# Optimization experiments

Measured on AMD Instinct MI355X. Metric: run time of the kernel, lower is better.

The kernel has to match this reference:

```python
import jax, jax.numpy as jnp
import numpy as np

B, S, E, H = 4, 2048, 2048, 16
HD = E // H  # 128
SCALE = 1.0 / float(np.sqrt(HD))


def setup_inputs() -> dict:
    key = jax.random.key(0)
    ks = jax.random.split(key, 9)
    std = 0.02
    return {
        "QKV": jax.random.normal(ks[0], (B, S, E), dtype=jnp.float32),
        "Wq": jax.random.normal(ks[1], (E, E), dtype=jnp.float32) * std,
        "bq": jnp.zeros((E,), dtype=jnp.float32),
        "Wk": jax.random.normal(ks[2], (E, E), dtype=jnp.float32) * std,
        "bk": jnp.zeros((E,), dtype=jnp.float32),
        "Wv": jax.random.normal(ks[3], (E, E), dtype=jnp.float32) * std,
        "bv": jnp.zeros((E,), dtype=jnp.float32),
        "Wo": jax.random.normal(ks[4], (E, E), dtype=jnp.float32) * std,
        "bo": jnp.zeros((E,), dtype=jnp.float32),
        "is_causal": 1,
    }


def _split_heads(x):
    # [B,S,E] -> [B,H,S,HD]
    return x.reshape(B, -1, H, HD).transpose(0, 2, 1, 3)


def reference(QKV, Wq, bq, Wk, bk, Wv, bv, Wo, bo, is_causal):
    # nn.Linear: y = x @ W.T + b
    Q = _split_heads(QKV @ Wq.T + bq)
    K = _split_heads(QKV @ Wk.T + bk)
    V = _split_heads(QKV @ Wv.T + bv)
    P = jnp.einsum("bhqd,bhkd->bhqk", Q, K) * SCALE
    # FAITHFUL: original masked_fill uses (ones_like(...) == 0) -> all-False
    # mask, so causal masking is a no-op regardless of is_causal.
    P = jax.nn.softmax(P, axis=-1)
    out = jnp.einsum("bhqk,bhkd->bhqd", P, V)
    out = out.transpose(0, 2, 1, 3).reshape(B, -1, E)  # [B,S,E]
    return out @ Wo.T + bo
```

## Files before the change

kernel.cpp:

```cpp
#include <hip/hip_runtime.h>
#include <stdint.h>

#define BB 4
#define SS 2048
#define EE 2048
#define HH 16
#define HD 128
#define QSCALE 0.1275174490044696f

typedef __attribute__((ext_vector_type(8))) short bf16x8;
typedef __attribute__((ext_vector_type(4))) float f32x4;

__device__ __forceinline__ unsigned short f2bf(float f) {
  union { float f; unsigned u; } v;
  v.f = f;
  unsigned r = (v.u + 0x7fffu + ((v.u >> 16) & 1u)) >> 16;
  return (unsigned short)r;
}
__device__ __forceinline__ float bf2f(unsigned short u) {
  union { unsigned u; float f; } v;
  v.u = ((unsigned)u) << 16;
  return v.f;
}

__device__ __forceinline__ void lds16(const void* g, void* l) {
  __builtin_amdgcn_global_load_lds(
      (__attribute__((address_space(1))) void*)(uintptr_t)g,
      (__attribute__((address_space(3))) void*)(uintptr_t)l,
      16, 0, 0);
}

__global__ void cvt_f32_bf16(const float* __restrict__ src,
                             unsigned short* __restrict__ dst, int n4) {
  int i = blockIdx.x * blockDim.x + threadIdx.x;
  if (i >= n4) return;
  float4 v = ((const float4*)src)[i];
  ushort4 o;
  o.x = f2bf(v.x); o.y = f2bf(v.y); o.z = f2bf(v.z); o.w = f2bf(v.w);
  ((ushort4*)dst)[i] = o;
}

__global__ void cvt_w3(const float* __restrict__ Wq,
                       const float* __restrict__ Wk,
                       const float* __restrict__ Wv,
                       unsigned short* __restrict__ dst, int n4each) {
  const int which = blockIdx.y;
  const float* src = (which == 0) ? Wq : (which == 1) ? Wk : Wv;
  unsigned short* d = dst + (size_t)which * 4194304;
  int i = blockIdx.x * blockDim.x + threadIdx.x;
  if (i >= n4each) return;
  float4 v = ((const float4*)src)[i];
  ushort4 o;
  o.x = f2bf(v.x); o.y = f2bf(v.y); o.z = f2bf(v.z); o.w = f2bf(v.w);
  ((ushort4*)d)[i] = o;
}

__device__ __forceinline__ void gemm_bt_core(const unsigned short* __restrict__ A,
                                             const unsigned short* __restrict__ Bm,
                                             unsigned short* As, unsigned short* Bs,
                                             int m0, int n0, int K, f32x4 acc[4][4]) {
  const int t = threadIdx.x;
  const int w = t >> 6;
  const int lr = t & 15;
  const int lg = (t & 63) >> 4;
  const int wm = (w >> 1) * 64;
  const int wn = (w & 1) * 64;

  const unsigned short* Ag0 = A + (size_t)(m0 + (t >> 2)) * K + (t & 3) * 8;
  const unsigned short* Ag1 = Ag0 + (size_t)64 * K;
  const unsigned short* Bg0 = Bm + (size_t)(n0 + (t >> 2)) * K + (t & 3) * 8;
  const unsigned short* Bg1 = Bg0 + (size_t)64 * K;
  char* AsB = (char*)As + (w * 64) * 16;
  char* BsB = (char*)Bs + (w * 64) * 16;

#pragma unroll
  for (int i = 0; i < 4; ++i)
#pragma unroll
    for (int j = 0; j < 4; ++j)
      acc[i][j] = (f32x4){0.f, 0.f, 0.f, 0.f};

  for (int kt = 0; kt < K; kt += 32) {
    lds16(Ag0 + kt, AsB);
    lds16(Ag1 + kt, AsB + 256 * 16);
    lds16(Bg0 + kt, BsB);
    lds16(Bg1 + kt, BsB + 256 * 16);
    __syncthreads();
    bf16x8 af[4], bf[4];
#pragma unroll
    for (int i = 0; i < 4; ++i)
      af[i] = *(const bf16x8*)(As + (wm + i * 16 + lr) * 32 + lg * 8);
#pragma unroll
    for (int j = 0; j < 4; ++j)
      bf[j] = *(const bf16x8*)(Bs + (wn + j * 16 + lr) * 32 + lg * 8);
#pragma unroll
    for (int i = 0; i < 4; ++i)
#pragma unroll
      for (int j = 0; j < 4; ++j)
        acc[i][j] = __builtin_amdgcn_mfma_f32_16x16x32_bf16(af[i], bf[j], acc[i][j], 0, 0, 0);
    __syncthreads();
  }
}

__global__ __launch_bounds__(256, 2)
void gemm_qkv(const unsigned short* __restrict__ X,
              const unsigned short* __restrict__ W,
              const float* __restrict__ bq,
              const float* __restrict__ bk,
              const float* __restrict__ bv,
              unsigned short* __restrict__ Qb,
              unsigned short* __restrict__ Kb,
              unsigned short* __restrict__ Vb) {
  __shared__ __align__(16) unsigned short As[128 * 32];
  __shared__ __align__(16) unsigned short Bs[128 * 32];
  const int m0 = blockIdx.y * 128;
  const int n0 = blockIdx.x * 128;
  f32x4 acc[4][4];
  gemm_bt_core(X, W, As, Bs, m0, n0, EE, acc);

  const int t = threadIdx.x;
  const int w = t >> 6;
  const int lr = t & 15;
  const int lg = (t & 63) >> 4;
  const int wm = (w >> 1) * 64;
  const int wn = (w & 1) * 64;

  const int region = n0 >> 11;
  unsigned short* Dst = (region == 0) ? Qb : (region == 1) ? Kb : Vb;
  const float* bp = (region == 0) ? bq : (region == 1) ? bk : bv;

  if (region == 2) {
#pragma unroll
    for (int i = 0; i < 4; ++i) {
      const int row0 = m0 + wm + i * 16 + lg * 4;
      const int b = row0 >> 11;
      const int s = row0 & 2047;
#pragma unroll
      for (int j = 0; j < 4; ++j) {
        const int c = (n0 + wn + j * 16 + lr) & 2047;
        const float bias = bp[c];
        const int h = c >> 7, hd = c & 127;
        const size_t base = ((size_t)(b * HH + h) * HD + hd) * SS + s;
#pragma unroll
        for (int re = 0; re < 4; ++re)
          Dst[base + re] = f2bf(acc[i][j][re] + bias);
      }
    }
  } else {
    const float osc = (region == 0) ? QSCALE : 1.0f;
#pragma unroll
    for (int i = 0; i < 4; ++i) {
      const int row0 = m0 + wm + i * 16 + lg * 4;
      const int b = row0 >> 11;
      const int s = row0 & 2047;
#pragma unroll
      for (int j = 0; j < 4; ++j) {
        const int c = (n0 + wn + j * 16 + lr) & 2047;
        const float bias = bp[c];
        const int h = c >> 7, hd = c & 127;
        const size_t base = ((size_t)(b * HH + h) * SS + s) * HD + hd;
#pragma unroll
        for (int re = 0; re < 4; ++re)
          Dst[base + (size_t)re * HD] = f2bf((acc[i][j][re] + bias) * osc);
      }
    }
  }
}

__global__ __launch_bounds__(256, 2)
void gemm_out(const unsigned short* __restrict__ A,
              const unsigned short* __restrict__ W,
              const float* __restrict__ bo,
              float* __restrict__ Out) {
  __shared__ __align__(16) unsigned short As[128 * 32];
  __shared__ __align__(16) unsigned short Bs[128 * 32];
  const int m0 = blockIdx.y * 128;
  const int n0 = blockIdx.x * 128;
  f32x4 acc[4][4];
  gemm_bt_core(A, W, As, Bs, m0, n0, EE, acc);

  const int t = threadIdx.x;
  const int w = t >> 6;
  const int lr = t & 15;
  const int lg = (t & 63) >> 4;
  const int wm = (w >> 1) * 64;
  const int wn = (w & 1) * 64;

#pragma unroll
  for (int i = 0; i < 4; ++i) {
    const int row0 = m0 + wm + i * 16 + lg * 4;
#pragma unroll
    for (int j = 0; j < 4; ++j) {
      const int col = n0 + wn + j * 16 + lr;
      const float bias = bo[col];
#pragma unroll
      for (int re = 0; re < 4; ++re)
        Out[(size_t)(row0 + re) * EE + col] = acc[i][j][re] + bias;
    }
  }
}

__global__ __launch_bounds__(256, 2)
void attn_mfma(const unsigned short* __restrict__ Qb,
               const unsigned short* __restrict__ Kb,
               const unsigned short* __restrict__ Vtb,
               unsigned short* __restrict__ At) {
  __shared__ __align__(16) char lds[81920];
  const int t = threadIdx.x;
  const int w = t >> 6;
  const int ln = t & 63;
  const int lr = ln & 15;
  const int lg = ln >> 4;
  char* Ps = lds + 65536 + w * 4096;

  const int bh = blockIdx.y;
  const int qw = blockIdx.x * 128 + w * 32;

  const unsigned short* Qh = Qb + (size_t)bh * SS * HD;
  const unsigned short* Kh = Kb + (size_t)bh * SS * HD;
  const unsigned short* Vh = Vtb + (size_t)bh * HD * SS;

  bf16x8 qfr[2][4];
#pragma unroll
  for (int qi = 0; qi < 2; ++qi)
#pragma unroll
    for (int ds = 0; ds < 4; ++ds)
      qfr[qi][ds] = *(const bf16x8*)(Qh + (size_t)(qw + qi * 16 + lr) * HD + ds * 32 + lg * 8);

  f32x4 acc[8][2];
#pragma unroll
  for (int df = 0; df < 8; ++df)
#pragma unroll
    for (int qi = 0; qi < 2; ++qi)
      acc[df][qi] = (f32x4){0.f, 0.f, 0.f, 0.f};
  float mrun[2] = {-3.0e38f, -3.0e38f};
  float lsum[2] = {0.f, 0.f};

#define STAGE_KV(kt, buf)                                                      \
  do {                                                                         \
    char* Kd = lds + (buf) * 32768;                                            \
    char* Vd = Kd + 16384;                                                     \
    _Pragma("unroll") for (int i = 0; i < 4; ++i) {                            \
      const int c = i * 256 + w * 64 + ln;                                     \
      const int row = c >> 4;                                                  \
      const int gch = (c & 15) ^ (row & 7);                                    \
      lds16(Kh + (size_t)((kt) + row) * HD + gch * 8,                          \
            Kd + (i * 256 + w * 64) * 16);                                     \
    }                                                                          \
    _Pragma("unroll") for (int i = 0; i < 4; ++i) {                            \
      const int c = i * 256 + w * 64 + ln;                                     \
      const int d = c >> 3;                                                    \
      const int kc = (c & 7) ^ (d & 7);                                        \
      lds16(Vh + (size_t)d * SS + (kt) + kc * 8,                               \
            Vd + (i * 256 + w * 64) * 16);                                     \
    }                                                                          \
  } while (0)

  STAGE_KV(0, 0);
  __syncthreads();

  int cur = 0;
  for (int kt = 0; kt < SS; kt += 64) {
    if (kt + 64 < SS) STAGE_KV(kt + 64, cur ^ 1);

    char* Ks = lds + cur * 32768;
    char* Vs = Ks + 16384;

    f32x4 st[4][2];
    __builtin_amdgcn_s_setprio(1);
#pragma unroll
    for (int kf = 0; kf < 4; ++kf) {
#pragma unroll
      for (int qi = 0; qi < 2; ++qi) st[kf][qi] = (f32x4){0.f, 0.f, 0.f, 0.f};
#pragma unroll
      for (int ds = 0; ds < 4; ++ds) {
        const int krow = kf * 16 + lr;
        bf16x8 kfr = *(const bf16x8*)(Ks + krow * 256 + (((ds * 4 + lg) ^ (krow & 7)) * 16));
#pragma unroll
        for (int qi = 0; qi < 2; ++qi)
          st[kf][qi] = __builtin_amdgcn_mfma_f32_16x16x32_bf16(kfr, qfr[qi][ds], st[kf][qi], 0, 0, 0);
      }
    }
    __builtin_amdgcn_s_setprio(0);

#pragma unroll
    for (int qi = 0; qi < 2; ++qi) {
      float tm = st[0][qi][0];
#pragma unroll
      for (int kf = 0; kf < 4; ++kf)
#pragma unroll
        for (int r = 0; r < 4; ++r) tm = fmaxf(tm, st[kf][qi][r]);
      tm = fmaxf(tm, __shfl_xor(tm, 16, 64));
      tm = fmaxf(tm, __shfl_xor(tm, 32, 64));
      if (!__all(tm <= mrun[qi] + 8.0f)) {
        const float mnew = fmaxf(mrun[qi], tm);
        const float alpha = __builtin_exp2f(mrun[qi] - mnew);
        mrun[qi] = mnew;
        lsum[qi] *= alpha;
#pragma unroll
        for (int df = 0; df < 8; ++df) {
          acc[df][qi][0] *= alpha; acc[df][qi][1] *= alpha;
          acc[df][qi][2] *= alpha; acc[df][qi][3] *= alpha;
        }
      }
      const float mcur = mrun[qi];
      float rs = 0.f;
      const int qrow = qi * 16 + lr;
#pragma unroll
      for (int kf = 0; kf < 4; ++kf) {
        const float p0 = __builtin_exp2f(st[kf][qi][0] - mcur);
        const float p1 = __builtin_exp2f(st[kf][qi][1] - mcur);
        const float p2 = __builtin_exp2f(st[kf][qi][2] - mcur);
        const float p3 = __builtin_exp2f(st[kf][qi][3] - mcur);
        rs += (p0 + p1) + (p2 + p3);
        ushort4 pk;
        pk.x = f2bf(p0); pk.y = f2bf(p1); pk.z = f2bf(p2); pk.w = f2bf(p3);
        const int k0 = kf * 16 + lg * 4;
        *(ushort4*)(Ps + qrow * 128 + (((k0 >> 3) ^ (qrow & 7)) * 16) + (k0 & 7) * 2) = pk;
      }
      lsum[qi] += rs;
    }

    bf16x8 pf[2][2];
#pragma unroll
    for (int ks = 0; ks < 2; ++ks)
#pragma unroll
      for (int qi = 0; qi < 2; ++qi) {
        const int qrow = qi * 16 + lr;
        pf[ks][qi] = *(const bf16x8*)(Ps + qrow * 128 + (((ks * 4 + lg) ^ (qrow & 7)) * 16));
      }
    __builtin_amdgcn_s_setprio(1);
#pragma unroll
    for (int df = 0; df < 8; ++df) {
#pragma unroll
      for (int ks = 0; ks < 2; ++ks) {
        const int drow = df * 16 + lr;
        bf16x8 vfr = *(const bf16x8*)(Vs + drow * 128 + (((ks * 4 + lg) ^ (drow & 7)) * 16));
#pragma unroll
        for (int qi = 0; qi < 2; ++qi)
          acc[df][qi] = __builtin_amdgcn_mfma_f32_16x16x32_bf16(vfr, pf[ks][qi], acc[df][qi], 0, 0, 0);
      }
    }
    __builtin_amdgcn_s_setprio(0);

    __syncthreads();
    cur ^= 1;
  }

  const int b = bh >> 4, h = bh & 15;
#pragma unroll
  for (int qi = 0; qi < 2; ++qi) {
    float l = lsum[qi];
    l += __shfl_xor(l, 16, 64);
    l += __shfl_xor(l, 32, 64);
    const float rl = 1.0f / l;
    const int s = qw + qi * 16 + lr;
    unsigned short* orow = At + ((size_t)(b * SS + s)) * EE + h * HD;
#pragma unroll
    for (int df = 0; df < 8; ++df)
#pragma unroll
      for (int r = 0; r < 4; ++r)
        orow[df * 16 + lg * 4 + r] = f2bf(acc[df][qi][r] * rl);
  }
}

extern "C" void kernel_launch(void* const* d_in, const int* in_sizes, int n_in,
                              void* d_out, int out_size, void* d_ws, size_t ws_size,
                              hipStream_t stream) {
  const float* QKV = (const float*)d_in[0];
  const float* Wq  = (const float*)d_in[1];
  const float* bq  = (const float*)d_in[2];
  const float* Wk  = (const float*)d_in[3];
  const float* bk  = (const float*)d_in[4];
  const float* Wv  = (const float*)d_in[5];
  const float* bv  = (const float*)d_in[6];
  const float* Wo  = (const float*)d_in[7];
  const float* bo  = (const float*)d_in[8];

  unsigned short* Xb = (unsigned short*)d_out;

  char* ws = (char*)d_ws;
  unsigned short* Wqkvb = (unsigned short*)(ws);
  unsigned short* Qb    = (unsigned short*)(ws + ( 24u << 20));
  unsigned short* Kb    = (unsigned short*)(ws + ( 56u << 20));
  unsigned short* Vb    = (unsigned short*)(ws + ( 88u << 20));
  unsigned short* At    = (unsigned short*)(ws + (120u << 20));
  unsigned short* Wob   = Wqkvb;

  cvt_f32_bf16<<<dim3(16384), dim3(256), 0, stream>>>(QKV, Xb, 4194304);
  cvt_w3<<<dim3(4096, 3), dim3(256), 0, stream>>>(Wq, Wk, Wv, Wqkvb, 1048576);

  gemm_qkv<<<dim3(48, 64), dim3(256), 0, stream>>>(Xb, Wqkvb, bq, bk, bv, Qb, Kb, Vb);
  attn_mfma<<<dim3(16, 64), dim3(256), 0, stream>>>(Qb, Kb, Vb, At);

  cvt_f32_bf16<<<dim3(4096), dim3(256), 0, stream>>>(Wo, Wob, 1048576);
  gemm_out<<<dim3(16, 64), dim3(256), 0, stream>>>(At, Wob, bo, (float*)d_out);
}
```

Baseline: 676.8 us.

## Rewrite projection GEMMs with 256x256 tiles, double-buffered swizzled LDS

Replaces the 128x128, single-buffered, K=32 GEMM core with a 256x256 tile, 512-thread core. It uses K=64 steps, an XOR-swizzled LDS layout, and double buffering, so global-to-LDS loads for the next tile overlap MFMA work on the current one. Each phase is split into four parts with barriers and setprio around the MFMA bursts. The goal is higher arithmetic intensity per byte loaded, fewer LDS bank conflicts and better latency hiding in the QKV and output projections. The trade-offs are 128 KB of LDS per block, one block per CU, and fewer blocks, which risks underfilling the GPU (768 and 256 blocks).

```diff
diff --git a/kernel.cpp b/kernel.cpp
--- a/kernel.cpp
+++ b/kernel.cpp
@@ -16,11 +16,6 @@
   v.f = f;
   unsigned r = (v.u + 0x7fffu + ((v.u >> 16) & 1u)) >> 16;
   return (unsigned short)r;
-}
-__device__ __forceinline__ float bf2f(unsigned short u) {
-  union { unsigned u; float f; } v;
-  v.u = ((unsigned)u) << 16;
-  return v.f;
 }
 
 __device__ __forceinline__ void lds16(const void* g, void* l) {
@@ -55,53 +50,104 @@
   ((ushort4*)d)[i] = o;
 }
 
-__device__ __forceinline__ void gemm_bt_core(const unsigned short* __restrict__ A,
-                                             const unsigned short* __restrict__ Bm,
-                                             unsigned short* As, unsigned short* Bs,
-                                             int m0, int n0, int K, f32x4 acc[4][4]) {
+__device__ __forceinline__ void gemm256_core(
+    const unsigned short* __restrict__ A,
+    const unsigned short* __restrict__ Bm,
+    char* lds, int m0, int n0, f32x4 acc[8][4]) {
   const int t = threadIdx.x;
   const int w = t >> 6;
-  const int lr = t & 15;
-  const int lg = (t & 63) >> 4;
-  const int wm = (w >> 1) * 64;
-  const int wn = (w & 1) * 64;
-
-  const unsigned short* Ag0 = A + (size_t)(m0 + (t >> 2)) * K + (t & 3) * 8;
-  const unsigned short* Ag1 = Ag0 + (size_t)64 * K;
-  const unsigned short* Bg0 = Bm + (size_t)(n0 + (t >> 2)) * K + (t & 3) * 8;
-  const unsigned short* Bg1 = Bg0 + (size_t)64 * K;
-  char* AsB = (char*)As + (w * 64) * 16;
-  char* BsB = (char*)Bs + (w * 64) * 16;
-
-#pragma unroll
-  for (int i = 0; i < 4; ++i)
-#pragma unroll
-    for (int j = 0; j < 4; ++j)
-      acc[i][j] = (f32x4){0.f, 0.f, 0.f, 0.f};
-
-  for (int kt = 0; kt < K; kt += 32) {
-    lds16(Ag0 + kt, AsB);
-    lds16(Ag1 + kt, AsB + 256 * 16);
-    lds16(Bg0 + kt, BsB);
-    lds16(Bg1 + kt, BsB + 256 * 16);
-    __syncthreads();
-    bf16x8 af[4], bf[4];
-#pragma unroll
-    for (int i = 0; i < 4; ++i)
-      af[i] = *(const bf16x8*)(As + (wm + i * 16 + lr) * 32 + lg * 8);
-#pragma unroll
-    for (int j = 0; j < 4; ++j)
-      bf[j] = *(const bf16x8*)(Bs + (wn + j * 16 + lr) * 32 + lg * 8);
-#pragma unroll
-    for (int i = 0; i < 4; ++i)
-#pragma unroll
-      for (int j = 0; j < 4; ++j)
-        acc[i][j] = __builtin_amdgcn_mfma_f32_16x16x32_bf16(af[i], bf[j], acc[i][j], 0, 0, 0);
-    __syncthreads();
+  const int ln = t & 63;
+  const int lr = ln & 15;
+  const int lg = ln >> 4;
+  const int wr = w >> 2;
+  const int wc = w & 3;
+
+  unsigned offs[4][2];
+  int dof[4][2];
+#pragma unroll
+  for (int h = 0; h < 2; ++h)
+#pragma unroll
+    for (int s = 0; s < 2; ++s) {
+      const int C = s * 512 + w * 64 + ln;
+      const int row = C >> 3;
+      const int kch = (C & 7) ^ (row & 7);
+      offs[h][s]     = (unsigned)(m0 + h * 128 + row) * EE + kch * 8;
+      offs[2 + h][s] = (unsigned)(n0 + h * 128 + row) * EE + kch * 8;
+      dof[h][s] = h * 16384 + (s * 512 + w * 64) * 16;
+      dof[2 + h][s] = 32768 + h * 16384 + (s * 512 + w * 64) * 16;
+    }
+
+#pragma unroll
+  for (int i = 0; i < 8; ++i)
+#pragma unroll
+    for (int j = 0; j < 4; ++j) acc[i][j] = (f32x4){0.f, 0.f, 0.f, 0.f};
+
+#pragma unroll
+  for (int q = 0; q < 4; ++q)
+#pragma unroll
+    for (int s = 0; s < 2; ++s)
+      lds16(((q < 2) ? A : Bm) + offs[q][s], lds + dof[q][s]);
+  __syncthreads();
+
+  const int cc0 = lg ^ (lr & 7);
+  const int cc1 = (4 + lg) ^ (lr & 7);
+  const int brbase = (wc & 1) * 64;
+
+  bf16x8 afr[4][2];
+  bf16x8 bfr[2][2][2];
+  int bufo = 0;
+  for (int kt = 0; kt < EE; kt += 64) {
+    char* cb = lds + bufo;
+    char* pb = lds + (bufo ^ 65536);
+    const char* Ard = cb + wr * 16384;
+    const char* Brd = cb + 32768 + (wc >> 1) * 16384;
+    const bool pre = (kt + 64 < EE);
+#pragma unroll
+    for (int ph = 0; ph < 4; ++ph) {
+      const int qm = ph >> 1, qn = ph & 1;
+      if (qn == 0) {
+#pragma unroll
+        for (int i = 0; i < 4; ++i) {
+          const int r = qm * 64 + i * 16 + lr;
+          afr[i][0] = *(const bf16x8*)(Ard + r * 128 + cc0 * 16);
+          afr[i][1] = *(const bf16x8*)(Ard + r * 128 + cc1 * 16);
+        }
+      }
+      if (ph < 2) {
+#pragma unroll
+        for (int j = 0; j < 2; ++j) {
+          const int r = brbase + ph * 32 + j * 16 + lr;
+          bfr[ph][j][0] = *(const bf16x8*)(Brd + r * 128 + cc0 * 16);
+          bfr[ph][j][1] = *(const bf16x8*)(Brd + r * 128 + cc1 * 16);
+        }
+      }
+      if (pre) {
+        lds16(((ph < 2) ? A : Bm) + (offs[ph][0] + (kt + 64)), pb + dof[ph][0]);
+        lds16(((ph < 2) ? A : Bm) + (offs[ph][1] + (kt + 64)), pb + dof[ph][1]);
+      }
+      __builtin_amdgcn_s_barrier();
+      __builtin_amdgcn_s_setprio(1);
+#pragma unroll
+      for (int i = 0; i < 4; ++i)
+#pragma unroll
+        for (int j = 0; j < 2; ++j) {
+          acc[qm * 4 + i][qn * 2 + j] = __builtin_amdgcn_mfma_f32_16x16x32_bf16(
+              afr[i][0], bfr[qn][j][0], acc[qm * 4 + i][qn * 2 + j], 0, 0, 0);
+          acc[qm * 4 + i][qn * 2 + j] = __builtin_amdgcn_mfma_f32_16x16x32_bf16(
+              afr[i][1], bfr[qn][j][1], acc[qm * 4 + i][qn * 2 + j], 0, 0, 0);
+        }
+      __builtin_amdgcn_s_setprio(0);
+      if (ph < 3) {
+        __builtin_amdgcn_s_barrier();
+      } else {
+        __syncthreads();
+      }
+    }
+    bufo ^= 65536;
   }
 }
 
-__global__ __launch_bounds__(256, 2)
+__global__ __launch_bounds__(512, 1)
 void gemm_qkv(const unsigned short* __restrict__ X,
               const unsigned short* __restrict__ W,
               const float* __restrict__ bq,
@@ -110,19 +156,18 @@
               unsigned short* __restrict__ Qb,
               unsigned short* __restrict__ Kb,
               unsigned short* __restrict__ Vb) {
-  __shared__ __align__(16) unsigned short As[128 * 32];
-  __shared__ __align__(16) unsigned short Bs[128 * 32];
-  const int m0 = blockIdx.y * 128;
-  const int n0 = blockIdx.x * 128;
-  f32x4 acc[4][4];
-  gemm_bt_core(X, W, As, Bs, m0, n0, EE, acc);
+  __shared__ __align__(16) char lds[131072];
+  const int m0 = blockIdx.y * 256;
+  const int n0 = blockIdx.x * 256;
+  f32x4 acc[8][4];
+  gemm256_core(X, W, lds, m0, n0, acc);
 
   const int t = threadIdx.x;
   const int w = t >> 6;
   const int lr = t & 15;
   const int lg = (t & 63) >> 4;
-  const int wm = (w >> 1) * 64;
-  const int wn = (w & 1) * 64;
+  const int wrm = (w >> 2) * 128;
+  const int wcn = (w & 3) * 64;
 
   const int region = n0 >> 11;
   unsigned short* Dst = (region == 0) ? Qb : (region == 1) ? Kb : Vb;
@@ -130,71 +175,70 @@
 
   if (region == 2) {
 #pragma unroll
-    for (int i = 0; i < 4; ++i) {
-      const int row0 = m0 + wm + i * 16 + lg * 4;
+    for (int mi = 0; mi < 8; ++mi) {
+      const int row0 = m0 + wrm + mi * 16 + lg * 4;
       const int b = row0 >> 11;
       const int s = row0 & 2047;
 #pragma unroll
-      for (int j = 0; j < 4; ++j) {
-        const int c = (n0 + wn + j * 16 + lr) & 2047;
+      for (int nj = 0; nj < 4; ++nj) {
+        const int c = (n0 + wcn + nj * 16 + lr) & 2047;
         const float bias = bp[c];
         const int h = c >> 7, hd = c & 127;
         const size_t base = ((size_t)(b * HH + h) * HD + hd) * SS + s;
 #pragma unroll
         for (int re = 0; re < 4; ++re)
-          Dst[base + re] = f2bf(acc[i][j][re] + bias);
+          Dst[base + re] = f2bf(acc[mi][nj][re] + bias);
       }
     }
   } else {
     const float osc = (region == 0) ? QSCALE : 1.0f;
 #pragma unroll
-    for (int i = 0; i < 4; ++i) {
-      const int row0 = m0 + wm + i * 16 + lg * 4;
+    for (int mi = 0; mi < 8; ++mi) {
+      const int row0 = m0 + wrm + mi * 16 + lg * 4;
       const int b = row0 >> 11;
       const int s = row0 & 2047;
 #pragma unroll
-      for (int j = 0; j < 4; ++j) {
-        const int c = (n0 + wn + j * 16 + lr) & 2047;
+      for (int nj = 0; nj < 4; ++nj) {
+        const int c = (n0 + wcn + nj * 16 + lr) & 2047;
         const float bias = bp[c];
         const int h = c >> 7, hd = c & 127;
         const size_t base = ((size_t)(b * HH + h) * SS + s) * HD + hd;
 #pragma unroll
         for (int re = 0; re < 4; ++re)
-          Dst[base + (size_t)re * HD] = f2bf((acc[i][j][re] + bias) * osc);
+          Dst[base + (size_t)re * HD] = f2bf((acc[mi][nj][re] + bias) * osc);
       }
     }
   }
 }
 
-__global__ __launch_bounds__(256, 2)
+__global__ __launch_bounds__(512, 1)
 void gemm_out(const unsigned short* __restrict__ A,
               const unsigned short* __restrict__ W,
               const float* __restrict__ bo,
               float* __restrict__ Out) {
-  __shared__ __align__(16) unsigned short As[128 * 32];
-  __shared__ __align__(16) unsigned short Bs[128 * 32];
-  const int m0 = blockIdx.y * 128;
-  const int n0 = blockIdx.x * 128;
-  f32x4 acc[4][4];
-  gemm_bt_core(A, W, As, Bs, m0, n0, EE, acc);
+  __shared__ __align__(16) char lds[131072];
+  const int m0 = blockIdx.y * 256;
+  const int n0 = blockIdx.x * 256;
+  f32x4 acc[8][4];
+  gemm256_core(A, W, lds, m0, n0, acc);
 
   const int t = threadIdx.x;
   const int w = t >> 6;
   const int lr = t & 15;
   const int lg = (t & 63) >> 4;
-  const int wm = (w >> 1) * 64;
-  const int wn = (w & 1) * 64;
-
-#pragma unroll
-  for (int i = 0; i < 4; ++i) {
-    const int row0 = m0 + wm + i * 16 + lg * 4;
-#pragma unroll
-    for (int j = 0; j < 4; ++j) {
-      const int col = n0 + wn + j * 16 + lr;
+  const int wrm = (w >> 2) * 128;
+  const int wcn = (w & 3) * 64;
+
+#pragma unroll
+  for (int mi = 0; mi < 8; ++mi) {
+    const int row0 = m0 + wrm + mi * 16 + lg * 4;
+#pragma unroll
+    for (int nj = 0; nj < 4; ++nj) {
+      const int col = n0 + wcn + nj * 16 + lr;
       const float bias = bo[col];
 #pragma unroll
       for (int re = 0; re < 4; ++re)
-        Out[(size_t)(row0 + re) * EE + col] = acc[i][j][re] + bias;
+        Out[(size_t)(row0 + re) * EE + col] = acc[mi][nj][re] + bias;
     }
   }
 }
@@ -389,9 +433,9 @@
   cvt_f32_bf16<<<dim3(16384), dim3(256), 0, stream>>>(QKV, Xb, 4194304);
   cvt_w3<<<dim3(4096, 3), dim3(256), 0, stream>>>(Wq, Wk, Wv, Wqkvb, 1048576);
 
-  gemm_qkv<<<dim3(48, 64), dim3(256), 0, stream>>>(Xb, Wqkvb, bq, bk, bv, Qb, Kb, Vb);
+  gemm_qkv<<<dim3(24, 32), dim3(512), 0, stream>>>(Xb, Wqkvb, bq, bk, bv, Qb, Kb, Vb);
   attn_mfma<<<dim3(16, 64), dim3(256), 0, stream>>>(Qb, Kb, Vb, At);
 
   cvt_f32_bf16<<<dim3(4096), dim3(256), 0, stream>>>(Wo, Wob, 1048576);
-  gemm_out<<<dim3(16, 64), dim3(256), 0, stream>>>(At, Wob, bo, (float*)d_out);
-}
+  gemm_out<<<dim3(8, 32), dim3(512), 0, stream>>>(At, Wob, bo, (float*)d_out);
+}
```

Result: faster. 614.3 us (-9.2%).
